# Optimization experiments

Measured on AMD Instinct MI355X. Metric: run time of the kernel, lower is better.

## Reference

```python
import jax, jax.numpy as jnp
from jax import lax
import numpy as np

DN = ('NCHW', 'OIHW', 'NCHW')
K = 3          # deformable kernel size
DG = 4         # deform groups
EXP = 4        # InvBottle expansion


def conv_offset(x, w1, w2, b2):
    """InvBottle with diff=True: depthwise-expanded 3x3 conv, diff correction, 1x1 conv."""
    B, C, H, W = x.shape
    _x = lax.conv_general_dilated(x, w1, (1, 1), ((1, 1), (1, 1)),
                                  dimension_numbers=DN, feature_group_count=C)  # [B,4C,H,W]
    # diff_conv: subtract grouped 1x1 conv with the kernel-summed weight
    wsum = w1.sum((2, 3)).reshape(1, EXP * C, 1, 1)          # [1,4C,1,1]
    xd = _x - jnp.repeat(x, EXP, axis=1) * wsum              # group g uses input channel g
    t = lax.conv_general_dilated(xd, w2, (1, 1), ((0, 0), (0, 0)), dimension_numbers=DN)
    return t + b2.reshape(1, -1, 1, 1)                       # [B,72,H,W]


def deform_depthwise(x, off, w, pad=1):
    """Depthwise DeformConv2d (groups=C, deform_groups=DG), stride=1, dilation=1."""
    B, C, H, W = x.shape
    Cg = C // DG
    off = off.reshape(B, DG, K * K, 2, H, W)                 # (dy, dx) interleaved per tap
    dy, dx = off[:, :, :, 0], off[:, :, :, 1]                # [B,DG,9,H,W]
    ky = (jnp.arange(K * K) // K).reshape(1, 1, K * K, 1, 1).astype(x.dtype)
    kx = (jnp.arange(K * K) % K).reshape(1, 1, K * K, 1, 1).astype(x.dtype)
    py = jnp.arange(H, dtype=x.dtype).reshape(1, 1, 1, H, 1) - pad + ky + dy
    px = jnp.arange(W, dtype=x.dtype).reshape(1, 1, 1, 1, W) - pad + kx + dx

    y0 = jnp.floor(py)
    x0 = jnp.floor(px)
    wy = py - y0
    wx = px - x0

    xg = x.reshape(B, DG, Cg, H * W)

    def gather(yy, xx):
        valid = ((yy >= 0) & (yy < H) & (xx >= 0) & (xx < W)).astype(x.dtype)
        yc = jnp.clip(yy, 0, H - 1).astype(jnp.int32)
        xc = jnp.clip(xx, 0, W - 1).astype(jnp.int32)
        idx = (yc * W + xc).reshape(B, DG, 1, K * K * H * W)
        v = jnp.take_along_axis(xg, jnp.broadcast_to(idx, (B, DG, Cg, K * K * H * W)), axis=3)
        return v.reshape(B, DG, Cg, K * K, H, W) * valid[:, :, None]

    val = (gather(y0, x0) * ((1 - wy) * (1 - wx))[:, :, None]
           + gather(y0, x0 + 1) * ((1 - wy) * wx)[:, :, None]
           + gather(y0 + 1, x0) * (wy * (1 - wx))[:, :, None]
           + gather(y0 + 1, x0 + 1) * (wy * wx)[:, :, None])   # [B,DG,Cg,9,H,W]

    val = val.reshape(B, C, K * K, H, W)
    return jnp.einsum('bckhw,ck->bchw', val, w.reshape(C, K * K))


def setup_inputs() -> dict:
    key = jax.random.key(0)
    ks = jax.random.split(key, 6)
    B, C, H, W = 2, 64, 192, 192
    x1 = jax.random.normal(ks[0], (B, C, H, W), jnp.float32)
    w_off1 = jax.random.normal(ks[1], (EXP * C, 1, K, K), jnp.float32) * 0.1
    w_off2 = jax.random.normal(ks[2], (DG * 2 * K * K, EXP * C, 1, 1), jnp.float32) * 0.1
    b_off2 = jax.random.normal(ks[3], (DG * 2 * K * K,), jnp.float32) * 0.1
    w_def = jax.random.normal(ks[4], (C, 1, K, K), jnp.float32) * 0.1
    w_out = jax.random.normal(ks[5], (C, C, 1, 1), jnp.float32) * 0.1
    return {'x1': x1, 'w_off1': w_off1, 'w_off2': w_off2, 'b_off2': b_off2,
            'w_def': w_def, 'w_out': w_out}


def reference(x1, w_off1, w_off2, b_off2, w_def, w_out):
    x2 = x1
    C = x1.shape[1]
    t = conv_offset(x1, w_off1, w_off2, b_off2)              # [B,72,H,W]
    y = deform_depthwise(x1, t, w_def)                       # DeformConv2d, groups=C
    # diff_conv against the deform conv's kernel-summed depthwise weight
    y = y - x2 * w_def.sum((1, 2, 3)).reshape(1, C, 1, 1)
    m = jnp.einsum('bchw,oc->bohw', y, w_out.reshape(w_out.shape[0], C))  # 1x1, no bias
    return (x1, m)
```

## Files before the change

### kernel.cpp

```cpp
#include <hip/hip_runtime.h>

#define BN   2
#define CN   64
#define HN   192
#define WN   192
#define HWN  36864
#define OCN  256
#define JCN  72
#define SN   32

#define DROWS 8
#define XH    17
#define XW    43
#define XRT   4
#define XCL   4
#define CI    12

#define PGRPS 2304

typedef __attribute__((ext_vector_type(8))) short bf16x8;
typedef __attribute__((ext_vector_type(8))) unsigned short u16x8;
typedef __attribute__((ext_vector_type(4))) float f32x4;

__device__ __forceinline__ unsigned short f2bf(float f) {
    union { float f; unsigned u; } v; v.f = f;
    unsigned r = v.u + 0x7fffu + ((v.u >> 16) & 1u);
    return (unsigned short)(r >> 16);
}

__global__ __launch_bounds__(256) void k_prep(const float* __restrict__ w2,
                                              const float* __restrict__ w_out,
                                              const float* __restrict__ w1,
                                              unsigned short* __restrict__ w2mf,
                                              unsigned short* __restrict__ w_outmf,
                                              float* __restrict__ w1p) {
    int idx = blockIdx.x * 256 + threadIdx.x;
    if (idx < 20480) {
        int j  = idx & 7;
        int l  = (idx >> 3) & 63;
        int ts = idx >> 9;
        int tm = ts >> 3, s = ts & 7;
        int jrow = tm * 16 + (l & 15);
        int k    = s * 32 + (l >> 4) * 8 + j;
        float v = (jrow < JCN) ? w2[jrow * OCN + k] : 0.f;
        w2mf[idx] = f2bf(v);
    } else if (idx < 24576) {
        int r  = idx - 20480;
        int j  = r & 7;
        int l  = (r >> 3) & 63;
        int ts = r >> 9;
        int tm = ts >> 1, s = ts & 1;
        int m  = tm * 16 + (l & 15);
        int k  = s * 32 + (l >> 4) * 8 + j;
        w_outmf[r] = f2bf(w_out[m * CN + k]);
    } else if (idx < 26624) {
        int r = idx - 24576;
        int o = r >> 3, kk = r & 7;
        int k = kk < 4 ? kk : kk + 1;
        w1p[r] = w1[o * 9 + k];
    }
}

__global__ __launch_bounds__(512, 4) void k_offsets(const float* __restrict__ x,
                                                    const float* __restrict__ w1p,
                                                    const unsigned short* __restrict__ w2mf,
                                                    const float* __restrict__ b2,
                                                    float* __restrict__ t_out,
                                                    float* __restrict__ x_copy) {
    __shared__ float red[4 * 64 * 21];

    const int f  = blockIdx.x + 3 * blockIdx.y + 576 * blockIdx.z;
    const int nn = (f & 7) * 144 + (f >> 3);
    const int bx = nn % 3;
    const int by = (nn / 3) % 192;
    const int bz = nn / 576;

    const int tid  = threadIdx.x;
    const int wave = tid >> 6;
    const int sgrp = wave >> 2;
    const int wv   = wave & 3;
    const int lane = tid & 63;
    const int q    = lane >> 4;
    const int n    = lane & 15;
    const int x0   = bx * 64;
    const int y    = by;
    const int b    = bz;
    const int xcol = x0 + wv * 16 + n;
    const float* xb = x + (size_t)b * CN * HWN;

    auto load_chunk = [&](int s, float (*ld)[9]) {
        #pragma unroll
        for (int cc = 0; cc < 2; ++cc) {
            int c = 8 * s + 2 * q + cc;
            const float* xp = xb + (size_t)c * HWN;
            #pragma unroll
            for (int k = 0; k < 9; ++k) {
                int ky = k / 3, kx = k - 3 * ky;
                int yy = y - 1 + ky, xx = xcol - 1 + kx;
                float v = 0.f;
                if ((unsigned)yy < (unsigned)HN && (unsigned)xx < (unsigned)WN)
                    v = xp[yy * WN + xx];
                ld[cc][k] = v;
            }
        }
    };

    f32x4 acc[5];
    #pragma unroll
    for (int t = 0; t < 5; ++t) acc[t] = (f32x4){0.f, 0.f, 0.f, 0.f};

    const bf16x8* ap = (const bf16x8*)w2mf + lane;

    #pragma unroll
    for (int sgi = 0; sgi < 2; ++sgi) {
        if (sgrp == sgi) {
            float lbuf[2][2][9];
            load_chunk(sgi * 4, lbuf[0]);
            #pragma unroll
            for (int ss = 0; ss < 4; ++ss) {
                const int s = sgi * 4 + ss;
                if (ss < 3) load_chunk(s + 1, lbuf[(ss + 1) & 1]);
                float (*ld)[9] = lbuf[ss & 1];

                float dd[2][8];
                #pragma unroll
                for (int cc = 0; cc < 2; ++cc) {
                    int c = 8 * s + 2 * q + cc;
                    float ctr = ld[cc][4];
                    x_copy[((size_t)b * CN + c) * HWN + y * WN + xcol] = ctr;
                    #pragma unroll
                    for (int kk = 0; kk < 8; ++kk) {
                        int k = kk < 4 ? kk : kk + 1;
                        dd[cc][kk] = ld[cc][k] - ctr;
                    }
                }

                bf16x8 bfr;
                const float4* wp = (const float4*)(w1p + (size_t)(s * 32 + q * 8) * 8);
                #pragma unroll
                for (int j = 0; j < 8; ++j) {
                    float4 wa = wp[2 * j];
                    float4 wb = wp[2 * j + 1];
                    const float* d = dd[j >> 2];
                    float a = wa.x * d[0] + wa.y * d[1] + wa.z * d[2] + wa.w * d[3]
                            + wb.x * d[4] + wb.y * d[5] + wb.z * d[6] + wb.w * d[7];
                    bfr[j] = (short)f2bf(a);
                }

                #pragma unroll
                for (int tm = 0; tm < 5; ++tm) {
                    bf16x8 af = ap[(tm * 8 + s) * 64];
                    acc[tm] = __builtin_amdgcn_mfma_f32_16x16x32_bf16(af, bfr, acc[tm], 0, 0, 0);
                }
            }
        }
    }

    float* rp = &red[(wv * 64 + lane) * 21];
    if (sgrp == 1) {
        #pragma unroll
        for (int tm = 0; tm < 5; ++tm)
            #pragma unroll
            for (int r = 0; r < 4; ++r)
                rp[tm * 4 + r] = acc[tm][r];
    }
    __syncthreads();
    if (sgrp == 0) {
        float* tb = t_out + (size_t)b * JCN * HWN + y * WN + x0 + wv * 16 + n;
        #pragma unroll
        for (int tm = 0; tm < 5; ++tm) {
            #pragma unroll
            for (int r = 0; r < 4; ++r) {
                int j = tm * 16 + q * 4 + r;
                if (j < JCN)
                    tb[(size_t)j * HWN] = acc[tm][r] + rp[tm * 4 + r] + b2[j];
            }
        }
    }
}

__device__ __forceinline__ float dsample(const float* __restrict__ p, int yi, int xi) {
    if ((unsigned)yi < (unsigned)HN && (unsigned)xi < (unsigned)WN)
        return p[yi * WN + xi];
    return 0.f;
}

__global__ __launch_bounds__(256, 4) void k_deform(const float* __restrict__ x,
                                                   const float* __restrict__ t_in,
                                                   const float* __restrict__ wdef,
                                                   unsigned short* __restrict__ y_out) {
    __shared__ float xs[XH * XW * CI];
    __shared__ float wks[9 * 8];
    __shared__ float wsums[8];

    const int f    = blockIdx.x + 6 * blockIdx.y + 144 * blockIdx.z;
    const int slot = f >> 3;
    const int xcd  = f & 7;
    const int tile = slot >> 1;
    const int cm   = slot & 1;
    const int zz   = 2 * xcd + cm;
    const int bx   = tile % 6;
    const int byy  = tile / 6;

    const int x0   = bx * SN;
    const int yr0  = byy * DROWS;
    const int b    = zz >> 3;
    const int chunk = zz & 7;
    const int g    = chunk >> 1;
    const int tid  = threadIdx.x;
    const int r    = tid >> 5;
    const int px   = tid & 31;
    const int row_lo = yr0 - XRT;
    const int col_lo = x0 - XCL;
    const float* xb = x + (size_t)b * CN * HWN;

    float dyr[9], dxr[9];
    {
        const float* tbp = t_in + ((size_t)b * JCN + g * 18) * HWN
                         + (yr0 + r) * WN + x0 + px;
        #pragma unroll
        for (int k = 0; k < 9; ++k) {
            dyr[k] = tbp[(size_t)(2 * k) * HWN];
            dxr[k] = tbp[(size_t)(2 * k + 1) * HWN];
        }
    }

    for (int idx = tid; idx < 8 * XH * XW; idx += 256) {
        int cc  = idx / (XH * XW);
        int rem = idx - cc * (XH * XW);
        int rr  = rem / XW;
        int col = rem - rr * XW;
        int yy  = row_lo + rr;
        int xx  = col_lo + col;
        float v = 0.f;
        if ((unsigned)yy < (unsigned)HN && (unsigned)xx < (unsigned)WN)
            v = xb[(size_t)(chunk * 8 + cc) * HWN + yy * WN + xx];
        xs[(rr * XW + col) * CI + cc] = v;
    }
    if (tid < 72) {
        int k = tid >> 3, cc = tid & 7;
        wks[tid] = wdef[(chunk * 8 + cc) * 9 + k];
    } else if (tid < 80) {
        int cc = tid - 72;
        float s = 0.f;
        #pragma unroll
        for (int k = 0; k < 9; ++k) s += wdef[(chunk * 8 + cc) * 9 + k];
        wsums[cc] = s;
    }
    __syncthreads();

    float acc[8];
    {
        const float* ctr = xs + ((XRT + r) * XW + XCL + px) * CI;
        f32x4 c0 = *(const f32x4*)ctr;
        f32x4 c1 = *(const f32x4*)(ctr + 4);
        f32x4 w0 = *(const f32x4*)&wsums[0];
        f32x4 w1 = *(const f32x4*)&wsums[4];
        #pragma unroll
        for (int i = 0; i < 4; ++i) {
            acc[i]     = -c0[i] * w0[i];
            acc[4 + i] = -c1[i] * w1[i];
        }
    }

    const float ry_basef = (float)(yr0 + r - 1);
    const float rx_basef = (float)(x0 + px - 1);

    #pragma unroll
    for (int k = 0; k < 9; ++k) {
        const int ky = k / 3, kx = k - 3 * ky;
        float py  = ry_basef + (float)ky + dyr[k];
        float pxf = rx_basef + (float)kx + dxr[k];
        float y0f = floorf(py), x0f = floorf(pxf);
        float wy = py - y0f, wx = pxf - x0f;
        int yi = (int)y0f, xi = (int)x0f;
        int ry = yi - row_lo, rx = xi - col_lo;
        float omwy = 1.f - wy, omwx = 1.f - wx;
        float w00 = omwy * omwx;
        float w01 = omwy * wx;
        float w10 = wy * omwx;
        float w11 = wy * wx;
        float4 wka = *(const float4*)&wks[k * 8];
        float4 wkb = *(const float4*)&wks[k * 8 + 4];
        if ((unsigned)ry < (XH - 1) && (unsigned)rx < (XW - 1)) {
            const float* p00 = xs + (ry * XW + rx) * CI;
            const float* p10 = p00 + XW * CI;
            f32x4 a0 = *(const f32x4*)p00;
            f32x4 a1 = *(const f32x4*)(p00 + 4);
            f32x4 b0 = *(const f32x4*)(p00 + CI);
            f32x4 b1 = *(const f32x4*)(p00 + CI + 4);
            f32x4 c0 = *(const f32x4*)p10;
            f32x4 c1 = *(const f32x4*)(p10 + 4);
            f32x4 d0 = *(const f32x4*)(p10 + CI);
            f32x4 d1 = *(const f32x4*)(p10 + CI + 4);
            #pragma unroll
            for (int i = 0; i < 4; ++i) {
                float bil0 = a0[i] * w00 + b0[i] * w01 + c0[i] * w10 + d0[i] * w11;
                float bil1 = a1[i] * w00 + b1[i] * w01 + c1[i] * w10 + d1[i] * w11;
                acc[i]     += (&wka.x)[i] * bil0;
                acc[4 + i] += (&wkb.x)[i] * bil1;
            }
        } else {
            float wkv[8] = {wka.x, wka.y, wka.z, wka.w, wkb.x, wkb.y, wkb.z, wkb.w};
            #pragma unroll
            for (int c = 0; c < 8; ++c) {
                const float* xp = xb + (size_t)(chunk * 8 + c) * HWN;
                float v00 = dsample(xp, yi,     xi);
                float v01 = dsample(xp, yi,     xi + 1);
                float v10 = dsample(xp, yi + 1, xi);
                float v11 = dsample(xp, yi + 1, xi + 1);
                float bil = v00 * w00 + v01 * w01 + v10 * w10 + v11 * w11;
                acc[c] += wkv[c] * bil;
            }
        }
    }

    u16x8 pk;
    #pragma unroll
    for (int c = 0; c < 8; ++c) pk[c] = f2bf(acc[c]);
    const int P = (yr0 + r) * (WN / 16) + ((x0 + px) >> 4);
    unsigned short* yo = y_out
        + ((((size_t)b * PGRPS + P) * 2 + (chunk >> 2)) * 4 + (chunk & 3)) * 128
        + (px & 15) * 8;
    *(u16x8*)yo = pk;
}

__global__ __launch_bounds__(256, 8) void k_final(const unsigned short* __restrict__ y_bf,
                                                  const unsigned short* __restrict__ womf,
                                                  float* __restrict__ m_out) {
    const int tid  = threadIdx.x;
    const int wv   = tid >> 6;
    const int lane = tid & 63;
    const int q    = lane >> 4;
    const int n    = lane & 15;
    const int yr   = blockIdx.y;
    const int b    = blockIdx.z;
    const int P    = yr * (WN / 16) + blockIdx.x * 4 + wv;

    const unsigned short* yp = y_bf + ((size_t)b * PGRPS + P) * 1024;
    bf16x8 bfr0 = *(const bf16x8*)(yp + (0 * 64 + q * 16 + n) * 8);
    bf16x8 bfr1 = *(const bf16x8*)(yp + (1 * 64 + q * 16 + n) * 8);

    const bf16x8* ap = (const bf16x8*)womf + lane;
    f32x4 acc[4];
    #pragma unroll
    for (int tm = 0; tm < 4; ++tm) acc[tm] = (f32x4){0.f, 0.f, 0.f, 0.f};
    #pragma unroll
    for (int tm = 0; tm < 4; ++tm) {
        acc[tm] = __builtin_amdgcn_mfma_f32_16x16x32_bf16(ap[(tm * 2 + 0) * 64], bfr0, acc[tm], 0, 0, 0);
        acc[tm] = __builtin_amdgcn_mfma_f32_16x16x32_bf16(ap[(tm * 2 + 1) * 64], bfr1, acc[tm], 0, 0, 0);
    }

    float* mb = m_out + (size_t)b * CN * HWN + yr * WN + blockIdx.x * 64 + wv * 16 + n;
    #pragma unroll
    for (int tm = 0; tm < 4; ++tm) {
        #pragma unroll
        for (int r = 0; r < 4; ++r)
            mb[(size_t)(tm * 16 + q * 4 + r) * HWN] = acc[tm][r];
    }
}

extern "C" void kernel_launch(void* const* d_in, const int* in_sizes, int n_in,
                              void* d_out, int out_size, void* d_ws, size_t ws_size,
                              hipStream_t stream) {
    const float* x1    = (const float*)d_in[0];
    const float* w_off1 = (const float*)d_in[1];
    const float* w_off2 = (const float*)d_in[2];
    const float* b_off2 = (const float*)d_in[3];
    const float* w_def = (const float*)d_in[4];
    const float* w_out = (const float*)d_in[5];

    float* out = (float*)d_out;
    const size_t n_x = (size_t)BN * CN * HWN;
    float* out_x1 = out;
    float* out_m  = out + n_x;

    char* ws0 = (char*)d_ws;
    unsigned short* w2mf   = (unsigned short*)ws0;
    unsigned short* w_outmf = (unsigned short*)(ws0 + 40960);
    float* w1p    = (float*)(ws0 + 49152);
    float* t_ws   = (float*)(ws0 + 57344);
    unsigned short* y_bf = (unsigned short*)(ws0 + 57344 + 21233664);

    k_prep<<<dim3(104), dim3(256), 0, stream>>>(w_off2, w_out, w_off1, w2mf, w_outmf, w1p);
    k_offsets<<<dim3(WN / 64, HN, BN), dim3(512), 0, stream>>>(x1, w1p, w2mf, b_off2,
                                                               t_ws, out_x1);
    k_deform<<<dim3(WN / SN, HN / DROWS, BN * 8), dim3(256), 0, stream>>>(x1, t_ws, w_def, y_bf);
    k_final<<<dim3(WN / 64, HN, BN), dim3(256), 0, stream>>>(y_bf, w_outmf, out_m);
}
```

Baseline: 158.4 us.

## Share center-column loads via lane shuffles and stage k_final output through LDS

In the offset-conv kernel, each lane now loads only the left and right columns of its 3x3 neighborhood. The center column comes from neighboring lanes through shuffles, with an edge-lane fallback, which cuts the global loads per channel from 9 to 6. In k_final, the MFMA accumulators are written to a padded shared-memory tile and then stored to global memory as contiguous float4 rows instead of scattered per-element stores. This adds shuffle, LDS and barrier overhead in exchange for fewer loads and better-coalesced output writes.

```diff
diff --git a/kernel.cpp b/kernel.cpp
--- a/kernel.cpp
+++ b/kernel.cpp
@@ -88,19 +88,22 @@
     const int xcol = x0 + wv * 16 + n;
     const float* xb = x + (size_t)b * CN * HWN;
 
-    auto load_chunk = [&](int s, float (*ld)[9]) {
+    auto load_chunk = [&](int s, float (*lL)[3], float (*lR)[3]) {
         #pragma unroll
         for (int cc = 0; cc < 2; ++cc) {
             int c = 8 * s + 2 * q + cc;
             const float* xp = xb + (size_t)c * HWN;
             #pragma unroll
-            for (int k = 0; k < 9; ++k) {
-                int ky = k / 3, kx = k - 3 * ky;
-                int yy = y - 1 + ky, xx = xcol - 1 + kx;
-                float v = 0.f;
-                if ((unsigned)yy < (unsigned)HN && (unsigned)xx < (unsigned)WN)
-                    v = xp[yy * WN + xx];
-                ld[cc][k] = v;
+            for (int ky = 0; ky < 3; ++ky) {
+                int yy = y - 1 + ky;
+                int xl = xcol - 1, xr = xcol + 1;
+                float vl = 0.f, vr = 0.f;
+                if ((unsigned)yy < (unsigned)HN && (unsigned)xl < (unsigned)WN)
+                    vl = xp[yy * WN + xl];
+                if ((unsigned)yy < (unsigned)HN && (unsigned)xr < (unsigned)WN)
+                    vr = xp[yy * WN + xr];
+                lL[cc][ky] = vl;
+                lR[cc][ky] = vr;
             }
         }
     };
@@ -114,25 +117,36 @@
     #pragma unroll
     for (int sgi = 0; sgi < 2; ++sgi) {
         if (sgrp == sgi) {
-            float lbuf[2][2][9];
-            load_chunk(sgi * 4, lbuf[0]);
+            float bufL[2][2][3], bufR[2][2][3];
+            load_chunk(sgi * 4, bufL[0], bufR[0]);
             #pragma unroll
             for (int ss = 0; ss < 4; ++ss) {
                 const int s = sgi * 4 + ss;
-                if (ss < 3) load_chunk(s + 1, lbuf[(ss + 1) & 1]);
-                float (*ld)[9] = lbuf[ss & 1];
+                if (ss < 3) load_chunk(s + 1, bufL[(ss + 1) & 1], bufR[(ss + 1) & 1]);
+                float (*lL)[3] = bufL[ss & 1];
+                float (*lR)[3] = bufR[ss & 1];
 
                 float dd[2][8];
                 #pragma unroll
                 for (int cc = 0; cc < 2; ++cc) {
+                    float ctr3[3];
+                    #pragma unroll
+                    for (int ky = 0; ky < 3; ++ky) {
+                        float cA = __shfl_down(lL[cc][ky], 1);
+                        float cB = __shfl_up(lR[cc][ky], 1);
+                        ctr3[ky] = (n == 15) ? cB : cA;
+                    }
+                    const float ctr = ctr3[1];
                     int c = 8 * s + 2 * q + cc;
-                    float ctr = ld[cc][4];
                     x_copy[((size_t)b * CN + c) * HWN + y * WN + xcol] = ctr;
-                    #pragma unroll
-                    for (int kk = 0; kk < 8; ++kk) {
-                        int k = kk < 4 ? kk : kk + 1;
-                        dd[cc][kk] = ld[cc][k] - ctr;
-                    }
+                    dd[cc][0] = lL[cc][0]  - ctr;
+                    dd[cc][1] = ctr3[0]    - ctr;
+                    dd[cc][2] = lR[cc][0]  - ctr;
+                    dd[cc][3] = lL[cc][1]  - ctr;
+                    dd[cc][4] = lR[cc][1]  - ctr;
+                    dd[cc][5] = lL[cc][2]  - ctr;
+                    dd[cc][6] = ctr3[2]    - ctr;
+                    dd[cc][7] = lR[cc][2]  - ctr;
                 }
 
                 bf16x8 bfr;
@@ -328,6 +342,8 @@
 __global__ __launch_bounds__(256, 8) void k_final(const unsigned short* __restrict__ y_bf,
                                                   const unsigned short* __restrict__ womf,
                                                   float* __restrict__ m_out) {
+    __shared__ float ms[64 * 68];
+
     const int tid  = threadIdx.x;
     const int wv   = tid >> 6;
     const int lane = tid & 63;
@@ -351,12 +367,22 @@
         acc[tm] = __builtin_amdgcn_mfma_f32_16x16x32_bf16(ap[(tm * 2 + 1) * 64], bfr1, acc[tm], 0, 0, 0);
     }
 
-    float* mb = m_out + (size_t)b * CN * HWN + yr * WN + blockIdx.x * 64 + wv * 16 + n;
-    #pragma unroll
-    for (int tm = 0; tm < 4; ++tm) {
+    #pragma unroll
+    for (int tm = 0; tm < 4; ++tm)
         #pragma unroll
         for (int r = 0; r < 4; ++r)
-            mb[(size_t)(tm * 16 + q * 4 + r) * HWN] = acc[tm][r];
+            ms[(tm * 16 + q * 4 + r) * 68 + wv * 16 + n] = acc[tm][r];
+    __syncthreads();
+
+    const int o  = tid >> 2;
+    const int sg = tid & 3;
+    float* mb = m_out + (size_t)b * CN * HWN + (size_t)o * HWN + yr * WN
+              + blockIdx.x * 64 + sg * 16;
+    const float* mr = &ms[o * 68 + sg * 16];
+    #pragma unroll
+    for (int i = 0; i < 4; ++i) {
+        float4 v = *(const float4*)(mr + 4 * i);
+        *(float4*)(mb + 4 * i) = v;
     }
 }
 
```

Result: slower. 166.0 us (+4.8%).

## Drop split-K across wave groups in k_offsets; one wave covers all channels

Applied to the files above, without the earlier changes.

The offset kernel used to split the 64-channel reduction across two groups of four waves, then merge partial accumulators through shared memory and a barrier. Now each block has 256 threads, and each wave loops over all 8 channel chunks with a triple-buffered prefetch of input taps. This removes the LDS reduction and the __syncthreads, at the cost of halving per-block parallelism and lengthening each wave's serial chain. Launch bounds change to (256,2) and may allow more registers.

```diff
diff --git a/kernel.cpp b/kernel.cpp
--- a/kernel.cpp
+++ b/kernel.cpp
@@ -61,14 +61,12 @@
     }
 }
 
-__global__ __launch_bounds__(512, 4) void k_offsets(const float* __restrict__ x,
+__global__ __launch_bounds__(256, 2) void k_offsets(const float* __restrict__ x,
                                                     const float* __restrict__ w1p,
                                                     const unsigned short* __restrict__ w2mf,
                                                     const float* __restrict__ b2,
                                                     float* __restrict__ t_out,
                                                     float* __restrict__ x_copy) {
-    __shared__ float red[4 * 64 * 21];
-
     const int f  = blockIdx.x + 3 * blockIdx.y + 576 * blockIdx.z;
     const int nn = (f & 7) * 144 + (f >> 3);
     const int bx = nn % 3;
@@ -76,16 +74,14 @@
     const int bz = nn / 576;
 
     const int tid  = threadIdx.x;
-    const int wave = tid >> 6;
-    const int sgrp = wave >> 2;
-    const int wv   = wave & 3;
+    const int wv   = tid >> 6;
     const int lane = tid & 63;
     const int q    = lane >> 4;
     const int n    = lane & 15;
-    const int x0   = bx * 64;
+    const int n0   = bx * 64 + wv * 16;
     const int y    = by;
     const int b    = bz;
-    const int xcol = x0 + wv * 16 + n;
+    const int xcol = n0 + n;
     const float* xb = x + (size_t)b * CN * HWN;
 
     auto load_chunk = [&](int s, float (*ld)[9]) {
@@ -111,70 +107,54 @@
 
     const bf16x8* ap = (const bf16x8*)w2mf + lane;
 
-    #pragma unroll
-    for (int sgi = 0; sgi < 2; ++sgi) {
-        if (sgrp == sgi) {
-            float lbuf[2][2][9];
-            load_chunk(sgi * 4, lbuf[0]);
+    float lbuf[3][2][9];
+    load_chunk(0, lbuf[0]);
+    load_chunk(1, lbuf[1]);
+    #pragma unroll
+    for (int s = 0; s < 8; ++s) {
+        if (s < 6) load_chunk(s + 2, lbuf[(s + 2) % 3]);
+        float (*ld)[9] = lbuf[s % 3];
+
+        float dd[2][8];
+        #pragma unroll
+        for (int cc = 0; cc < 2; ++cc) {
+            int c = 8 * s + 2 * q + cc;
+            float ctr = ld[cc][4];
+            x_copy[((size_t)b * CN + c) * HWN + y * WN + xcol] = ctr;
             #pragma unroll
-            for (int ss = 0; ss < 4; ++ss) {
-                const int s = sgi * 4 + ss;
-                if (ss < 3) load_chunk(s + 1, lbuf[(ss + 1) & 1]);
-                float (*ld)[9] = lbuf[ss & 1];
-
-                float dd[2][8];
-                #pragma unroll
-                for (int cc = 0; cc < 2; ++cc) {
-                    int c = 8 * s + 2 * q + cc;
-                    float ctr = ld[cc][4];
-                    x_copy[((size_t)b * CN + c) * HWN + y * WN + xcol] = ctr;
-                    #pragma unroll
-                    for (int kk = 0; kk < 8; ++kk) {
-                        int k = kk < 4 ? kk : kk + 1;
-                        dd[cc][kk] = ld[cc][k] - ctr;
-                    }
-                }
-
-                bf16x8 bfr;
-                const float4* wp = (const float4*)(w1p + (size_t)(s * 32 + q * 8) * 8);
-                #pragma unroll
-                for (int j = 0; j < 8; ++j) {
-                    float4 wa = wp[2 * j];
-                    float4 wb = wp[2 * j + 1];
-                    const float* d = dd[j >> 2];
-                    float a = wa.x * d[0] + wa.y * d[1] + wa.z * d[2] + wa.w * d[3]
-                            + wb.x * d[4] + wb.y * d[5] + wb.z * d[6] + wb.w * d[7];
-                    bfr[j] = (short)f2bf(a);
-                }
-
-                #pragma unroll
-                for (int tm = 0; tm < 5; ++tm) {
-                    bf16x8 af = ap[(tm * 8 + s) * 64];
-                    acc[tm] = __builtin_amdgcn_mfma_f32_16x16x32_bf16(af, bfr, acc[tm], 0, 0, 0);
-                }
+            for (int kk = 0; kk < 8; ++kk) {
+                int k = kk < 4 ? kk : kk + 1;
+                dd[cc][kk] = ld[cc][k] - ctr;
             }
         }
-    }
-
-    float* rp = &red[(wv * 64 + lane) * 21];
-    if (sgrp == 1) {
-        #pragma unroll
-        for (int tm = 0; tm < 5; ++tm)
-            #pragma unroll
-            for (int r = 0; r < 4; ++r)
-                rp[tm * 4 + r] = acc[tm][r];
-    }
-    __syncthreads();
-    if (sgrp == 0) {
-        float* tb = t_out + (size_t)b * JCN * HWN + y * WN + x0 + wv * 16 + n;
+
+        bf16x8 bfr;
+        const float4* wp = (const float4*)(w1p + (size_t)(s * 32 + q * 8) * 8);
+        #pragma unroll
+        for (int j = 0; j < 8; ++j) {
+            float4 wa = wp[2 * j];
+            float4 wb = wp[2 * j + 1];
+            const float* d = dd[j >> 2];
+            float a = wa.x * d[0] + wa.y * d[1] + wa.z * d[2] + wa.w * d[3]
+                    + wb.x * d[4] + wb.y * d[5] + wb.z * d[6] + wb.w * d[7];
+            bfr[j] = (short)f2bf(a);
+        }
+
         #pragma unroll
         for (int tm = 0; tm < 5; ++tm) {
-            #pragma unroll
-            for (int r = 0; r < 4; ++r) {
-                int j = tm * 16 + q * 4 + r;
-                if (j < JCN)
-                    tb[(size_t)j * HWN] = acc[tm][r] + rp[tm * 4 + r] + b2[j];
-            }
+            bf16x8 af = ap[(tm * 8 + s) * 64];
+            acc[tm] = __builtin_amdgcn_mfma_f32_16x16x32_bf16(af, bfr, acc[tm], 0, 0, 0);
+        }
+    }
+
+    float* tb = t_out + (size_t)b * JCN * HWN + y * WN + n0 + n;
+    #pragma unroll
+    for (int tm = 0; tm < 5; ++tm) {
+        #pragma unroll
+        for (int r = 0; r < 4; ++r) {
+            int j = tm * 16 + q * 4 + r;
+            if (j < JCN)
+                tb[(size_t)j * HWN] = acc[tm][r] + b2[j];
         }
     }
 }
@@ -383,7 +363,7 @@
     unsigned short* y_bf = (unsigned short*)(ws0 + 57344 + 21233664);
 
     k_prep<<<dim3(104), dim3(256), 0, stream>>>(w_off2, w_out, w_off1, w2mf, w_outmf, w1p);
-    k_offsets<<<dim3(WN / 64, HN, BN), dim3(512), 0, stream>>>(x1, w1p, w2mf, b_off2,
+    k_offsets<<<dim3(WN / 64, HN, BN), dim3(256), 0, stream>>>(x1, w1p, w2mf, b_off2,
                                                                t_ws, out_x1);
     k_deform<<<dim3(WN / SN, HN / DROWS, BN * 8), dim3(256), 0, stream>>>(x1, t_ws, w_def, y_bf);
     k_final<<<dim3(WN / 64, HN, BN), dim3(256), 0, stream>>>(y_bf, w_outmf, out_m);
```

Measured after the change: 162.2 us. 2.4% more time.
